# Kernel tuning notes

Measured on AMD Instinct MI355X. Metric: run time of the kernel, lower is better.

Reference implementation:

```python
import jax, jax.numpy as jnp
import numpy as np

EMBED = 512
HEADS = 1
HEAD_DIM = EMBED // HEADS  # 512 (heads must be 1 for the original torch code to run)
N, S = 4, 4096


def setup_inputs() -> dict:
    key = jax.random.key(0)
    ks = jax.random.split(key, 9)
    scale = 1.0 / np.sqrt(EMBED)
    return {
        "values": jax.random.normal(ks[0], (N, 1, S, EMBED), dtype=jnp.float32),
        "keys": jax.random.normal(ks[1], (N, 1, S, EMBED), dtype=jnp.float32),
        "query": jax.random.normal(ks[2], (N, 1, S, EMBED), dtype=jnp.float32),
        "mask": jax.random.randint(ks[3], (N, 1, S, S), 0, 2, dtype=jnp.int32),
        "Wv": jax.random.normal(ks[4], (EMBED, EMBED), dtype=jnp.float32) * scale,
        "Wk": jax.random.normal(ks[5], (EMBED, EMBED), dtype=jnp.float32) * scale,
        "Wq": jax.random.normal(ks[6], (EMBED, EMBED), dtype=jnp.float32) * scale,
        "Wo": jax.random.normal(ks[7], (EMBED, EMBED), dtype=jnp.float32) * scale,
        "bo": jnp.zeros((EMBED,), dtype=jnp.float32),
    }


def reference(values, keys, query, mask, Wv, Wk, Wq, Wo, bo):
    n = query.shape[0]
    q_len = query.shape[2]
    # reshape(N, -1, heads, head_dim); inputs are [N, 1, S, E] -> [N, S, H, Dh]
    v = values.reshape(n, -1, HEADS, HEAD_DIM)
    k = keys.reshape(n, -1, HEADS, HEAD_DIM)
    q = query.reshape(n, -1, HEADS, HEAD_DIM)
    # per-module linear projections (nn.Linear: y = x @ W.T)
    v = jnp.einsum('nlhd,ed->nlhe', v, Wv)
    k = jnp.einsum('nlhd,ed->nlhe', k, Wk)
    q = jnp.einsum('nqhd,ed->nqhe', q, Wq)
    # full [N, H, Q, K] score matrix, as in the original
    energy = jnp.einsum('nqhd,nkhd->nhqk', q, k)
    energy = jnp.where(mask == 0, jnp.float32(-1e20), energy)
    attn = jax.nn.softmax(energy / np.sqrt(HEAD_DIM), axis=3)
    out = jnp.einsum('nhql,nlhd->nqhd', attn, v).reshape(n, q_len, HEADS * HEAD_DIM)
    return out @ Wo.T + bo
```

## Files before the change

### kernel.cpp

```cpp
#include <hip/hip_runtime.h>

typedef __bf16 bf16x8 __attribute__((ext_vector_type(8)));
typedef __bf16 bf16x4 __attribute__((ext_vector_type(4)));
typedef float f32x4 __attribute__((ext_vector_type(4)));
typedef float f32x16 __attribute__((ext_vector_type(16)));

#define MFMA16(a, b, c) __builtin_amdgcn_mfma_f32_16x16x32_bf16((a), (b), (c), 0, 0, 0)
#define MFMA32(a, b, c) __builtin_amdgcn_mfma_f32_32x32x16_bf16((a), (b), (c), 0, 0, 0)

static constexpr int SEQ = 4096;
static constexpr int DIM = 512;

typedef __attribute__((address_space(3))) void lds_void;
typedef __attribute__((address_space(1))) const void gbl_void;

__device__ __forceinline__ void glds16(const void* g, void* l) {
    __builtin_amdgcn_global_load_lds((gbl_void*)g, (lds_void*)l, 16, 0, 0);
}

__device__ __forceinline__ bf16x8 cvt8f(const float* __restrict__ p) {
    float4 f0 = *(const float4*)p;
    float4 f1 = *(const float4*)(p + 4);
    bf16x8 v;
    v[0] = (__bf16)f0.x; v[1] = (__bf16)f0.y; v[2] = (__bf16)f0.z; v[3] = (__bf16)f0.w;
    v[4] = (__bf16)f1.x; v[5] = (__bf16)f1.y; v[6] = (__bf16)f1.z; v[7] = (__bf16)f1.w;
    return v;
}

__global__ __launch_bounds__(256)
void cvt_f32_bf16(const float* __restrict__ in, __bf16* __restrict__ out) {
    const size_t i = ((size_t)blockIdx.x * 256 + threadIdx.x) * 8;
    *(bf16x8*)(out + i) = cvt8f(in + i);
}

__global__ __launch_bounds__(256)
void convert_w(const float* __restrict__ wq, const float* __restrict__ wk,
               const float* __restrict__ wv, const float* __restrict__ wo,
               __bf16* __restrict__ out)
{
    const int z = blockIdx.y;
    const float* src = (z == 0) ? wq : (z == 1) ? wk : (z == 2) ? wv : wo;
    __bf16* dst = out + (size_t)z * DIM * DIM;
    const int i = (blockIdx.x * 256 + threadIdx.x) * 8;
    *(bf16x8*)(dst + i) = cvt8f(src + i);
}

template <bool TRANS>
__global__ __launch_bounds__(256, 3)
void gemm_bf16(const __bf16* __restrict__ Ap, const __bf16* __restrict__ Bp,
               __bf16* __restrict__ Cp)
{
    __shared__ __align__(16) char smem[128 * 132 * 2];
    __bf16* As = (__bf16*)smem;
    __bf16* Bs = (__bf16*)(smem + 16384);

    const int tid  = threadIdx.x;
    const int wave = tid >> 6;
    const int lane = tid & 63;
    const int quad = lane >> 4;
    const int l16  = lane & 15;
    const int m0 = blockIdx.x * 128;
    const int n0 = blockIdx.y * 128;
    const int wm = (wave >> 1) * 64;
    const int wn = (wave & 1) * 64;

    f32x4 acc[4][4] = {};

    for (int k0 = 0; k0 < DIM; k0 += 64) {
        #pragma unroll
        for (int i = 0; i < 4; i++) {
            const int j = wave * 4 + i;
            const int c = j * 64 + lane;
            const int row = c >> 3, c8 = c & 7;
            glds16(Ap + (size_t)(m0 + row) * DIM + k0 + c8 * 8, &As[j * 512]);
            glds16(Bp + (size_t)(n0 + row) * DIM + k0 + c8 * 8, &Bs[j * 512]);
        }
        __syncthreads();
        #pragma unroll
        for (int kk = 0; kk < 2; kk++) {
            bf16x8 af[4], bg[4];
            #pragma unroll
            for (int mt = 0; mt < 4; mt++)
                af[mt] = *(const bf16x8*)&As[(wm + mt * 16 + l16) * 64 + kk * 32 + quad * 8];
            #pragma unroll
            for (int nt = 0; nt < 4; nt++)
                bg[nt] = *(const bf16x8*)&Bs[(wn + nt * 16 + l16) * 64 + kk * 32 + quad * 8];
            #pragma unroll
            for (int mt = 0; mt < 4; mt++)
                #pragma unroll
                for (int nt = 0; nt < 4; nt++)
                    acc[mt][nt] = MFMA16(af[mt], bg[nt], acc[mt][nt]);
        }
        __syncthreads();
    }

    if (!TRANS) {
        #pragma unroll
        for (int mt = 0; mt < 4; mt++)
            #pragma unroll
            for (int nt = 0; nt < 4; nt++)
                #pragma unroll
                for (int r = 0; r < 4; r++)
                    Cp[(size_t)(m0 + wm + mt * 16 + quad * 4 + r) * DIM
                       + n0 + wn + nt * 16 + l16] = (__bf16)acc[mt][nt][r];
    } else {
        __bf16* Tt = (__bf16*)smem;
        #pragma unroll
        for (int mt = 0; mt < 4; mt++)
            #pragma unroll
            for (int nt = 0; nt < 4; nt++)
                #pragma unroll
                for (int r = 0; r < 4; r++)
                    Tt[(wm + mt * 16 + quad * 4 + r) * 132 + wn + nt * 16 + l16]
                        = (__bf16)acc[mt][nt][r];
        __syncthreads();
        const int nb  = m0 >> 12;
        const int s0m = m0 & 4095;
        const int d   = tid >> 1;
        const int sh  = (tid & 1) * 64;
        __bf16* dst = Cp + (size_t)nb * DIM * SEQ + (size_t)(n0 + d) * SEQ + s0m + sh;
        #pragma unroll
        for (int i = 0; i < 8; i++) {
            bf16x8 vv;
            #pragma unroll
            for (int e = 0; e < 8; e++) vv[e] = Tt[(sh + i * 8 + e) * 132 + d];
            *(bf16x8*)(dst + i * 8) = vv;
        }
    }
}

__global__ __launch_bounds__(256, 3)
void gemm_out(const __bf16* __restrict__ Ap, const __bf16* __restrict__ Bp,
              float* __restrict__ Cp, const float* __restrict__ bias)
{
    __shared__ __align__(16) __bf16 As[128 * 64];
    __shared__ __align__(16) __bf16 Bs[128 * 64];
    const int tid  = threadIdx.x;
    const int wave = tid >> 6;
    const int lane = tid & 63;
    const int quad = lane >> 4;
    const int l16  = lane & 15;
    const int m0 = blockIdx.x * 128;
    const int n0 = blockIdx.y * 128;
    const int wm = (wave >> 1) * 64;
    const int wn = (wave & 1) * 64;

    f32x4 acc[4][4] = {};

    for (int k0 = 0; k0 < DIM; k0 += 64) {
        #pragma unroll
        for (int i = 0; i < 4; i++) {
            const int j = wave * 4 + i;
            const int c = j * 64 + lane;
            const int row = c >> 3, c8 = c & 7;
            glds16(Ap + (size_t)(m0 + row) * DIM + k0 + c8 * 8, &As[j * 512]);
            glds16(Bp + (size_t)(n0 + row) * DIM + k0 + c8 * 8, &Bs[j * 512]);
        }
        __syncthreads();
        #pragma unroll
        for (int kk = 0; kk < 2; kk++) {
            bf16x8 af[4], bg[4];
            #pragma unroll
            for (int mt = 0; mt < 4; mt++)
                af[mt] = *(const bf16x8*)&As[(wm + mt * 16 + l16) * 64 + kk * 32 + quad * 8];
            #pragma unroll
            for (int nt = 0; nt < 4; nt++)
                bg[nt] = *(const bf16x8*)&Bs[(wn + nt * 16 + l16) * 64 + kk * 32 + quad * 8];
            #pragma unroll
            for (int mt = 0; mt < 4; mt++)
                #pragma unroll
                for (int nt = 0; nt < 4; nt++)
                    acc[mt][nt] = MFMA16(af[mt], bg[nt], acc[mt][nt]);
        }
        __syncthreads();
    }
    #pragma unroll
    for (int mt = 0; mt < 4; mt++)
        #pragma unroll
        for (int nt = 0; nt < 4; nt++)
            #pragma unroll
            for (int r = 0; r < 4; r++) {
                const int col = n0 + wn + nt * 16 + l16;
                Cp[(size_t)(m0 + wm + mt * 16 + quad * 4 + r) * DIM + col]
                    = acc[mt][nt][r] + bias[col];
            }
}

#define MKC(v, r4) ((r4) == 0 ? (v).x : (r4) == 1 ? (v).y : (r4) == 2 ? (v).z : (v).w)
#define WAITVM(n)  asm volatile("s_waitcnt vmcnt(" #n ")" ::: "memory")
#define WAITLGKM() asm volatile("s_waitcnt lgkmcnt(0)" ::: "memory")
#define BARRIER()  { __builtin_amdgcn_s_barrier(); __builtin_amdgcn_sched_barrier(0); }

__global__ __launch_bounds__(512, 1)
void flash_attn(__bf16* __restrict__ Qp, const __bf16* __restrict__ Kp,
                const __bf16* __restrict__ Vt, const int* __restrict__ mask)
{
    constexpr float SCALE = 0.044194173824159216f;

    __shared__ __bf16 KQ[3 * 20480];
    __shared__ __bf16 P[64 * 256];
    __shared__ float pmax[8 * 66];
    __shared__ float psum[8 * 66];

    const int bid  = blockIdx.x;
    const int n    = bid & 3;
    const int q0   = (bid >> 2) * 64;
    const int tid  = threadIdx.x;
    const int w    = tid >> 6;
    const int lane = tid & 63;
    const int l32  = lane & 31;
    const int half = lane >> 5;
    const int r8   = lane >> 3;
    const int c8   = lane & 7;
    const int gc   = c8 ^ r8;

    const __bf16* Qb = Qp + (size_t)n * SEQ * DIM;
    const __bf16* Kb = Kp + (size_t)n * SEQ * DIM;
    const __bf16* Vb = Vt + (size_t)n * DIM * SEQ;
    const int*    Mb = mask + (size_t)n * SEQ * SEQ;
    __bf16*       AO = Qp + (size_t)n * SEQ * DIM;

    auto stageK = [&](int slot, int k0, int dc) {
        __bf16* dst = &KQ[slot * 20480];
        #pragma unroll
        for (int i = 0; i < 4; i++) {
            const int R = (i * 8 + w) * 8 + r8;
            glds16(Kb + (size_t)(k0 + R) * DIM + dc * 64 + gc * 8,
                   &dst[(i * 8 + w) * 512]);
        }
    };
    auto stageV = [&](int slot, int k0, int vc) {
        __bf16* dst = &KQ[slot * 20480];
        const int h = vc >> 2, kc2 = vc & 3;
        #pragma unroll
        for (int i = 0; i < 4; i++) {
            const int R = (i * 8 + w) * 8 + r8;
            glds16(Vb + (size_t)(h * 256 + R) * SEQ + k0 + kc2 * 64 + gc * 8,
                   &dst[(i * 8 + w) * 512]);
        }
    };
    auto stageQ = [&](int slot, int dc) {
        glds16(Qb + (size_t)(q0 + w * 8 + r8) * DIM + dc * 64 + gc * 8,
               &KQ[slot * 20480 + 16384 + w * 512]);
    };

    float m0 = -__builtin_inff(), m1 = -__builtin_inff();
    float l0 = 0.f, l1 = 0.f;
    f32x16 o00 = {}, o01 = {}, o10 = {}, o11 = {};

    stageK(0, 0, 0); stageQ(0, 0);
    stageK(1, 0, 1); stageQ(1, 1);
    int cur = 0;

    #pragma unroll 1
    for (int j = 0; j < 16; j++) {
        const int k0 = j * 256;

        int4 mk0[4], mk1[4];
        {
            const int* mp0 = Mb + (size_t)(q0 + l32) * SEQ + k0 + 32 * w + 4 * half;
            const int* mp1 = mp0 + (size_t)32 * SEQ;
            #pragma unroll
            for (int g = 0; g < 4; g++) {
                mk0[g] = *(const int4*)(mp0 + 8 * g);
                mk1[g] = *(const int4*)(mp1 + 8 * g);
            }
        }

        f32x16 s0 = {}, s1 = {};
        #pragma unroll 1
        for (int dc = 0; dc < 8; dc++) {
            if (dc < 2)      WAITVM(13);
            else if (dc < 7) WAITVM(5);
            else             WAITVM(4);
            BARRIER();
            const int s2 = (cur >= 1) ? cur - 1 : cur + 2;
            if (dc < 6)      { stageK(s2, k0, dc + 2); stageQ(s2, dc + 2); }
            else if (dc == 6)  stageV(s2, k0, 0);
            else               stageV(s2, k0, 1);

            const __bf16* Kc = &KQ[cur * 20480];
            const __bf16* Qc = Kc + 16384;
            __builtin_amdgcn_s_setprio(1);
            #pragma unroll
            for (int ks = 0; ks < 4; ks++) {
                const int ch = (2 * ks + half) ^ (l32 & 7);
                bf16x8 a  = *(const bf16x8*)&Kc[(32 * w + l32) * 64 + ch * 8];
                bf16x8 b0 = *(const bf16x8*)&Qc[l32 * 64 + ch * 8];
                bf16x8 b1 = *(const bf16x8*)&Qc[(32 + l32) * 64 + ch * 8];
                s0 = MFMA32(a, b0, s0);
                s1 = MFMA32(a, b1, s1);
            }
            __builtin_amdgcn_s_setprio(0);
            if (dc == 7) {
                float mx0 = s0[0], mx1 = s1[0];
                #pragma unroll
                for (int r = 1; r < 16; r++) { mx0 = fmaxf(mx0, s0[r]); mx1 = fmaxf(mx1, s1[r]); }
                mx0 = fmaxf(mx0, __shfl_xor(mx0, 32));
                mx1 = fmaxf(mx1, __shfl_xor(mx1, 32));
                if (half == 0) pmax[w * 66 + l32]      = mx0;
                else           pmax[w * 66 + 32 + l32] = mx1;
            }
            cur = (cur < 2) ? cur + 1 : 0;
        }

        WAITLGKM();
        BARRIER();

        float mp0v = pmax[l32], mp1v = pmax[32 + l32];
        #pragma unroll
        for (int w2 = 1; w2 < 8; w2++) {
            mp0v = fmaxf(mp0v, pmax[w2 * 66 + l32]);
            mp1v = fmaxf(mp1v, pmax[w2 * 66 + 32 + l32]);
        }
        const float mn0 = fmaxf(m0, mp0v * SCALE);
        const float mn1 = fmaxf(m1, mp1v * SCALE);
        const float a0 = __expf(m0 - mn0);
        const float a1 = __expf(m1 - mn1);
        m0 = mn0; m1 = mn1;
        #pragma unroll
        for (int r = 0; r < 16; r++) {
            o00[r] *= a0; o10[r] *= a0;
            o01[r] *= a1; o11[r] *= a1;
        }

        float ls0 = 0.f, ls1 = 0.f;
        #pragma unroll
        for (int g = 0; g < 4; g++) {
            bf16x4 pv0, pv1;
            #pragma unroll
            for (int r4 = 0; r4 < 4; r4++) {
                const int r = g * 4 + r4;
                float p0 = __expf(s0[r] * SCALE - mn0);
                float p1 = __expf(s1[r] * SCALE - mn1);
                p0 = MKC(mk0[g], r4) ? p0 : 0.f;
                p1 = MKC(mk1[g], r4) ? p1 : 0.f;
                ls0 += p0; ls1 += p1;
                pv0[r4] = (__bf16)p0;
                pv1[r4] = (__bf16)p1;
            }
            const int c  = 4 * w + g;
            const int cp = (c & 24) | ((c & 7) ^ (l32 & 7));
            *(bf16x4*)&P[l32 * 256 + cp * 8 + 4 * half]        = pv0;
            *(bf16x4*)&P[(32 + l32) * 256 + cp * 8 + 4 * half] = pv1;
        }
        ls0 += __shfl_xor(ls0, 32);
        ls1 += __shfl_xor(ls1, 32);
        if (half == 0) psum[w * 66 + l32]      = ls0;
        else           psum[w * 66 + 32 + l32] = ls1;

        WAITVM(4);
        WAITLGKM();
        BARRIER();

        auto computeV = [&](int slot, int vc) {
            const __bf16* Vc = &KQ[slot * 20480];
            const int kc2 = vc & 3;
            __builtin_amdgcn_s_setprio(1);
            #pragma unroll
            for (int ks = 0; ks < 4; ks++) {
                const int ca = (2 * ks + half) ^ (l32 & 7);
                bf16x8 a = *(const bf16x8*)&Vc[(32 * w + l32) * 64 + ca * 8];
                const int ck = kc2 * 8 + 2 * ks + half;
                const int cp = (ck & 24) | ((ck & 7) ^ (l32 & 7));
                bf16x8 b0 = *(const bf16x8*)&P[l32 * 256 + cp * 8];
                bf16x8 b1 = *(const bf16x8*)&P[(32 + l32) * 256 + cp * 8];
                if (vc < 4) { o00 = MFMA32(a, b0, o00); o01 = MFMA32(a, b1, o01); }
                else        { o10 = MFMA32(a, b0, o10); o11 = MFMA32(a, b1, o11); }
            }
            __builtin_amdgcn_s_setprio(0);
        };

        {
            const int s2 = (cur >= 1) ? cur - 1 : cur + 2;
            stageV(s2, k0, 2);
            float ss0 = 0.f, ss1 = 0.f;
            #pragma unroll
            for (int w2 = 0; w2 < 8; w2++) {
                ss0 += psum[w2 * 66 + l32];
                ss1 += psum[w2 * 66 + 32 + l32];
            }
            l0 = l0 * a0 + ss0;
            l1 = l1 * a1 + ss1;
            computeV(cur, 0);
            cur = (cur < 2) ? cur + 1 : 0;
        }

        #pragma unroll 1
        for (int vc = 1; vc < 8; vc++) {
            if (vc < 7) WAITVM(4);
            else if (j < 15) WAITVM(5);
            else WAITVM(0);
            BARRIER();
            const int s2 = (cur >= 1) ? cur - 1 : cur + 2;
            if (vc < 6)        stageV(s2, k0, vc + 2);
            else if (vc == 6) { if (j < 15) { stageK(s2, k0 + 256, 0); stageQ(s2, 0); } }
            else              { if (j < 15) { stageK(s2, k0 + 256, 1); stageQ(s2, 1); } }
            computeV(cur, vc);
            cur = (cur < 2) ? cur + 1 : 0;
        }
    }

    const float li0 = 1.f / l0, li1 = 1.f / l1;
    __bf16* ao0 = AO + (size_t)(q0 + l32) * DIM;
    __bf16* ao1 = AO + (size_t)(q0 + 32 + l32) * DIM;
    #pragma unroll
    for (int h = 0; h < 2; h++) {
        #pragma unroll
        for (int g = 0; g < 4; g++) {
            bf16x4 v00, v01;
            #pragma unroll
            for (int r4 = 0; r4 < 4; r4++) {
                const int r = g * 4 + r4;
                v00[r4] = (__bf16)((h ? o10[r] : o00[r]) * li0);
                v01[r4] = (__bf16)((h ? o11[r] : o01[r]) * li1);
            }
            const int d = h * 256 + 32 * w + g * 8 + 4 * half;
            *(bf16x4*)&ao0[d] = v00;
            *(bf16x4*)&ao1[d] = v01;
        }
    }
}

extern "C" void kernel_launch(void* const* d_in, const int* in_sizes, int n_in,
                              void* d_out, int out_size, void* d_ws, size_t ws_size,
                              hipStream_t stream)
{
    const float* values = (const float*)d_in[0];
    const float* keys   = (const float*)d_in[1];
    const float* query  = (const float*)d_in[2];
    const int*   mask   = (const int*)d_in[3];
    const float* Wv = (const float*)d_in[4];
    const float* Wk = (const float*)d_in[5];
    const float* Wq = (const float*)d_in[6];
    const float* Wo = (const float*)d_in[7];
    const float* bo = (const float*)d_in[8];
    float* out = (float*)d_out;

    char* ws = (char*)d_ws;
    __bf16* Qp  = (__bf16*)(ws);
    __bf16* Kp  = (__bf16*)(ws + (16u << 20));
    __bf16* Vt  = (__bf16*)(ws + (32u << 20));
    __bf16* Abf = (__bf16*)(ws + (48u << 20));
    __bf16* wbf = (__bf16*)(ws + (64u << 20));

    const int M = 4 * SEQ;
    const dim3 gg(M / 128, DIM / 128);

    convert_w<<<dim3(128, 4), 256, 0, stream>>>(Wq, Wk, Wv, Wo, wbf);

    cvt_f32_bf16<<<4096, 256, 0, stream>>>(query, Abf);
    gemm_bf16<false><<<gg, 256, 0, stream>>>(Abf, wbf + 0 * DIM * DIM, Qp);

    cvt_f32_bf16<<<4096, 256, 0, stream>>>(keys, Abf);
    gemm_bf16<false><<<gg, 256, 0, stream>>>(Abf, wbf + 1 * DIM * DIM, Kp);

    cvt_f32_bf16<<<4096, 256, 0, stream>>>(values, Abf);
    gemm_bf16<true><<<gg, 256, 0, stream>>>(Abf, wbf + 2 * DIM * DIM, Vt);

    flash_attn<<<256, 512, 0, stream>>>(Qp, Kp, Vt, mask);

    gemm_out<<<gg, 256, 0, stream>>>(Qp , wbf + 3 * DIM * DIM, out, bo);
}
```

Measured before the change: 820.3 us.

## Fuse fp32-to-bf16 input conversion into a single batched QKV projection GEMM

```diff
diff --git a/kernel.cpp b/kernel.cpp
--- a/kernel.cpp
+++ b/kernel.cpp
@@ -25,12 +25,6 @@
     v[0] = (__bf16)f0.x; v[1] = (__bf16)f0.y; v[2] = (__bf16)f0.z; v[3] = (__bf16)f0.w;
     v[4] = (__bf16)f1.x; v[5] = (__bf16)f1.y; v[6] = (__bf16)f1.z; v[7] = (__bf16)f1.w;
     return v;
-}
-
-__global__ __launch_bounds__(256)
-void cvt_f32_bf16(const float* __restrict__ in, __bf16* __restrict__ out) {
-    const size_t i = ((size_t)blockIdx.x * 256 + threadIdx.x) * 8;
-    *(bf16x8*)(out + i) = cvt8f(in + i);
 }
 
 __global__ __launch_bounds__(256)
@@ -45,11 +39,17 @@
     *(bf16x8*)(dst + i) = cvt8f(src + i);
 }
 
-template <bool TRANS>
 __global__ __launch_bounds__(256, 3)
-void gemm_bf16(const __bf16* __restrict__ Ap, const __bf16* __restrict__ Bp,
-               __bf16* __restrict__ Cp)
+void gemm_qkv(const float* __restrict__ Aq, const float* __restrict__ Ak,
+              const float* __restrict__ Av, const __bf16* __restrict__ Wb,
+              __bf16* __restrict__ Qp, __bf16* __restrict__ Kp,
+              __bf16* __restrict__ Vtp)
 {
+    const int z = blockIdx.z;
+    const float* Ap = (z == 0) ? Aq : (z == 1) ? Ak : Av;
+    const __bf16* Bp = Wb + (size_t)z * DIM * DIM;
+    __bf16* Cp = (z == 0) ? Qp : (z == 1) ? Kp : Vtp;
+
     __shared__ __align__(16) char smem[128 * 132 * 2];
     __bf16* As = (__bf16*)smem;
     __bf16* Bs = (__bf16*)(smem + 16384);
@@ -70,10 +70,11 @@
         #pragma unroll
         for (int i = 0; i < 4; i++) {
             const int j = wave * 4 + i;
-            const int c = j * 64 + lane;
-            const int row = c >> 3, c8 = c & 7;
-            glds16(Ap + (size_t)(m0 + row) * DIM + k0 + c8 * 8, &As[j * 512]);
+            const int t = j * 64 + lane;
+            const int row = t >> 3, c8 = t & 7;
             glds16(Bp + (size_t)(n0 + row) * DIM + k0 + c8 * 8, &Bs[j * 512]);
+            *(bf16x8*)&As[t * 8] =
+                cvt8f(Ap + (size_t)(m0 + row) * DIM + k0 + c8 * 8);
         }
         __syncthreads();
         #pragma unroll
@@ -94,7 +95,7 @@
         __syncthreads();
     }
 
-    if (!TRANS) {
+    if (z < 2) {
         #pragma unroll
         for (int mt = 0; mt < 4; mt++)
             #pragma unroll
@@ -105,6 +106,7 @@
                        + n0 + wn + nt * 16 + l16] = (__bf16)acc[mt][nt][r];
     } else {
         __bf16* Tt = (__bf16*)smem;
+        __syncthreads();
         #pragma unroll
         for (int mt = 0; mt < 4; mt++)
             #pragma unroll
@@ -189,7 +191,7 @@
 #define MKC(v, r4) ((r4) == 0 ? (v).x : (r4) == 1 ? (v).y : (r4) == 2 ? (v).z : (v).w)
 #define WAITVM(n)  asm volatile("s_waitcnt vmcnt(" #n ")" ::: "memory")
 #define WAITLGKM() asm volatile("s_waitcnt lgkmcnt(0)" ::: "memory")
-#define BARRIER()  { __builtin_amdgcn_s_barrier(); __builtin_amdgcn_sched_barrier(0); }
+#define BARRIER()  asm volatile("s_barrier" ::: "memory")
 
 __global__ __launch_bounds__(512, 1)
 void flash_attn(__bf16* __restrict__ Qp, const __bf16* __restrict__ Kp,
@@ -441,24 +443,17 @@
     __bf16* Qp  = (__bf16*)(ws);
     __bf16* Kp  = (__bf16*)(ws + (16u << 20));
     __bf16* Vt  = (__bf16*)(ws + (32u << 20));
-    __bf16* Abf = (__bf16*)(ws + (48u << 20));
-    __bf16* wbf = (__bf16*)(ws + (64u << 20));
+    __bf16* wbf = (__bf16*)(ws + (48u << 20));
 
     const int M = 4 * SEQ;
-    const dim3 gg(M / 128, DIM / 128);
 
     convert_w<<<dim3(128, 4), 256, 0, stream>>>(Wq, Wk, Wv, Wo, wbf);
 
-    cvt_f32_bf16<<<4096, 256, 0, stream>>>(query, Abf);
-    gemm_bf16<false><<<gg, 256, 0, stream>>>(Abf, wbf + 0 * DIM * DIM, Qp);
-
-    cvt_f32_bf16<<<4096, 256, 0, stream>>>(keys, Abf);
-    gemm_bf16<false><<<gg, 256, 0, stream>>>(Abf, wbf + 1 * DIM * DIM, Kp);
-
-    cvt_f32_bf16<<<4096, 256, 0, stream>>>(values, Abf);
-    gemm_bf16<true><<<gg, 256, 0, stream>>>(Abf, wbf + 2 * DIM * DIM, Vt);
+    gemm_qkv<<<dim3(M / 128, DIM / 128, 3), 256, 0, stream>>>(
+        query, keys, values, wbf, Qp, Kp, Vt);
 
     flash_attn<<<256, 512, 0, stream>>>(Qp, Kp, Vt, mask);
 
-    gemm_out<<<gg, 256, 0, stream>>>(Qp , wbf + 3 * DIM * DIM, out, bo);
-}
+    gemm_out<<<dim3(M / 128, DIM / 128), 256, 0, stream>>>(
+        Qp , wbf + 3 * DIM * DIM, out, bo);
+}
```

Measured after the change: 811.1 us. About the same (-1.1%).
